# Kernel tuning notes

Measured on AMD Instinct MI355X. Metric: run time of the kernel, lower is better.

## Reference

```python
import jax, jax.numpy as jnp
import numpy as np

N = 100000   # num_nodes
E = 1250000  # num_edges
IN = 64
HID = 64
OUT = 64
LN_EPS = 1e-5


def _gcn_conv(x, src, dst, W, b, n):
    # PyG GCNConv: add self-loops, symmetric deg^{-1/2} normalization, then linear.
    h = x @ W  # (N, out)
    deg = jax.ops.segment_sum(jnp.ones(src.shape[0], h.dtype), dst, num_segments=n) + 1.0  # +1 self-loop
    dinv = jax.lax.rsqrt(deg)
    norm = dinv[src] * dinv[dst]  # (E,)
    out = jax.ops.segment_sum(h[src] * norm[:, None], dst, num_segments=n)
    out = out + h * (dinv * dinv)[:, None]  # self-loop message
    return out + b


def _sage_conv(x, src, dst, Wl, bl, Wr, n):
    # PyG SAGEConv(aggr='mean'): lin_l(mean_{j in N(i)} x_j) + lin_r(x_i); bias only in lin_l.
    cnt = jax.ops.segment_sum(jnp.ones(src.shape[0], x.dtype), dst, num_segments=n)
    agg = jax.ops.segment_sum(x[src], dst, num_segments=n) / jnp.maximum(cnt, 1.0)[:, None]
    return agg @ Wl + bl + x @ Wr


def _layer_norm(x, g, b):
    mu = jnp.mean(x, axis=-1, keepdims=True)
    var = jnp.var(x, axis=-1, keepdims=True)
    return (x - mu) * jax.lax.rsqrt(var + LN_EPS) * g + b


def setup_inputs() -> dict:
    key = jax.random.key(0)
    ks = jax.random.split(key, 16)
    def w(k, shape):
        fan_in = shape[0]
        return (jax.random.normal(k, shape, jnp.float32) / np.sqrt(fan_in)).astype(jnp.float32)
    x = jax.random.normal(ks[0], (N, IN), jnp.float32)
    edge_index = jax.random.randint(ks[1], (2, E), 0, N, dtype=jnp.int64)
    return {
        "x": x,
        "edge_index": edge_index,
        "gcn_w1": w(ks[2], (IN, HID)), "gcn_b1": jnp.zeros((HID,), jnp.float32),
        "gcn_w2": w(ks[3], (HID, OUT)), "gcn_b2": jnp.zeros((OUT,), jnp.float32),
        "sage_wl1": w(ks[4], (IN, HID)), "sage_bl1": jnp.zeros((HID,), jnp.float32),
        "sage_wr1": w(ks[5], (IN, HID)),
        "sage_wl2": w(ks[6], (HID, OUT)), "sage_bl2": jnp.zeros((OUT,), jnp.float32),
        "sage_wr2": w(ks[7], (HID, OUT)),
        "gcn_ln_g": jnp.ones((OUT,), jnp.float32), "gcn_ln_b": jnp.zeros((OUT,), jnp.float32),
        "sage_ln_g": jnp.ones((OUT,), jnp.float32), "sage_ln_b": jnp.zeros((OUT,), jnp.float32),
        "proj_w": w(ks[8], (2 * OUT, OUT)), "proj_b": jnp.zeros((OUT,), jnp.float32),
    }


def reference(x, edge_index, gcn_w1, gcn_b1, gcn_w2, gcn_b2,
              sage_wl1, sage_bl1, sage_wr1, sage_wl2, sage_bl2, sage_wr2,
              gcn_ln_g, gcn_ln_b, sage_ln_g, sage_ln_b, proj_w, proj_b):
    src, dst = edge_index[0], edge_index[1]
    n = x.shape[0]
    # GCN branch (dropout p=0 / eval -> identity)
    g = jax.nn.relu(_gcn_conv(x, src, dst, gcn_w1, gcn_b1, n))
    g = _gcn_conv(g, src, dst, gcn_w2, gcn_b2, n)
    # SAGE branch
    s = jax.nn.relu(_sage_conv(x, src, dst, sage_wl1, sage_bl1, sage_wr1, n))
    s = _sage_conv(s, src, dst, sage_wl2, sage_bl2, sage_wr2, n)
    # Norm + projected-concat fusion
    g = _layer_norm(g, gcn_ln_g, gcn_ln_b)
    s = _layer_norm(s, sage_ln_g, sage_ln_b)
    cat = jnp.concatenate([g, s], axis=-1)  # (N, 2*OUT)
    return cat @ proj_w + proj_b
```

## Files before the change

### kernel.cpp

```cpp
#include <hip/hip_runtime.h>


#define SCAN_CHUNK 2048

typedef __attribute__((ext_vector_type(8))) short short8;
typedef __attribute__((ext_vector_type(4))) short short4v;
typedef __attribute__((ext_vector_type(4))) float floatx4;

__device__ __forceinline__ unsigned short f2bf(float f) {
    unsigned int u = __float_as_uint(f);
    unsigned int r = u + 0x7FFFu + ((u >> 16) & 1u);
    return (unsigned short)(r >> 16);
}
__device__ __forceinline__ float bf2f(unsigned short h) {
    return __uint_as_float(((unsigned int)h) << 16);
}

__global__ void k_count(const int* __restrict__ ei, int E, int* __restrict__ cnt,
                        int* __restrict__ rank) {
    int i = blockIdx.x * blockDim.x + threadIdx.x;
    int e = i * 4;
    if (e + 4 <= E) {
        int4 d = *(const int4*)&ei[E + e];
        int4 r;
        r.x = atomicAdd(&cnt[d.x], 1);
        r.y = atomicAdd(&cnt[d.y], 1);
        r.z = atomicAdd(&cnt[d.z], 1);
        r.w = atomicAdd(&cnt[d.w], 1);
        *(int4*)&rank[e] = r;
    } else {
        for (int j = e; j < E; ++j) rank[j] = atomicAdd(&cnt[ei[E + j]], 1);
    }
}

__global__ void k_scan_reduce(const int* __restrict__ cnt, int N, int* __restrict__ blockSums) {
    __shared__ int lds[256];
    int base = blockIdx.x * SCAN_CHUNK;
    int t = threadIdx.x;
    int s = 0;
    for (int j = 0; j < 8; ++j) {
        int idx = base + t * 8 + j;
        if (idx < N) s += cnt[idx];
    }
    lds[t] = s;
    __syncthreads();
    for (int d = 128; d > 0; d >>= 1) {
        if (t < d) lds[t] += lds[t + d];
        __syncthreads();
    }
    if (t == 0) blockSums[blockIdx.x] = lds[0];
}

__global__ void k_scan_spine(int* __restrict__ blockSums, int B) {
    if (threadIdx.x == 0 && blockIdx.x == 0) {
        int run = 0;
        for (int b = 0; b < B; ++b) { int v = blockSums[b]; blockSums[b] = run; run += v; }
    }
}

__global__ void k_scan_write(const int* __restrict__ cnt, int N,
                             const int* __restrict__ blockSums,
                             int* __restrict__ offs, float* __restrict__ dinv) {
    __shared__ int lds[256];
    int base = blockIdx.x * SCAN_CHUNK;
    int t = threadIdx.x;
    int v[8];
    int s = 0;
    for (int j = 0; j < 8; ++j) {
        int idx = base + t * 8 + j;
        v[j] = (idx < N) ? cnt[idx] : 0;
        s += v[j];
    }
    lds[t] = s;
    __syncthreads();
    for (int d = 1; d < 256; d <<= 1) {
        int x = (t >= d) ? lds[t - d] : 0;
        __syncthreads();
        lds[t] += x;
        __syncthreads();
    }
    int excl = (t == 0) ? 0 : lds[t - 1];
    int run = blockSums[blockIdx.x] + excl;
    for (int j = 0; j < 8; ++j) {
        int idx = base + t * 8 + j;
        if (idx < N) {
            offs[idx] = run;
            run += v[j];
            dinv[idx] = rsqrtf((float)v[j] + 1.0f);
        }
    }
}

__global__ void k_fill(const int* __restrict__ ei, int E, const int* __restrict__ offs,
                       const int* __restrict__ rank, int* __restrict__ csr) {
    int i = blockIdx.x * blockDim.x + threadIdx.x;
    int e = i * 4;
    if (e + 4 <= E) {
        int4 s = *(const int4*)&ei[e];
        int4 d = *(const int4*)&ei[E + e];
        int4 r = *(const int4*)&rank[e];
        csr[offs[d.x] + r.x] = s.x;
        csr[offs[d.y] + r.y] = s.y;
        csr[offs[d.z] + r.z] = s.z;
        csr[offs[d.w] + r.w] = s.w;
    } else {
        for (int j = e; j < E; ++j) csr[offs[ei[E + j]] + rank[j]] = ei[j];
    }
}

__global__ void k_xtobf16(const float* __restrict__ x, unsigned short* __restrict__ xb, int total) {
    int i = blockIdx.x * blockDim.x + threadIdx.x;
    int e = i * 8;
    if (e + 8 <= total) {
        float4 a = *(const float4*)&x[e];
        float4 b = *(const float4*)&x[e + 4];
        short8 o;
        o[0] = (short)f2bf(a.x); o[1] = (short)f2bf(a.y);
        o[2] = (short)f2bf(a.z); o[3] = (short)f2bf(a.w);
        o[4] = (short)f2bf(b.x); o[5] = (short)f2bf(b.y);
        o[6] = (short)f2bf(b.z); o[7] = (short)f2bf(b.w);
        *(short8*)&xb[e] = o;
    } else {
        for (int j = e; j < total; ++j) xb[j] = f2bf(x[j]);
    }
}

__device__ __forceinline__ void xor_reduce8(float4& a, float4& b) {
    a.x += __shfl_xor(a.x, 16, 64); a.y += __shfl_xor(a.y, 16, 64);
    a.z += __shfl_xor(a.z, 16, 64); a.w += __shfl_xor(a.w, 16, 64);
    b.x += __shfl_xor(b.x, 16, 64); b.y += __shfl_xor(b.y, 16, 64);
    b.z += __shfl_xor(b.z, 16, 64); b.w += __shfl_xor(b.w, 16, 64);
    a.x += __shfl_xor(a.x, 32, 64); a.y += __shfl_xor(a.y, 32, 64);
    a.z += __shfl_xor(a.z, 32, 64); a.w += __shfl_xor(a.w, 32, 64);
    b.x += __shfl_xor(b.x, 32, 64); b.y += __shfl_xor(b.y, 32, 64);
    b.z += __shfl_xor(b.z, 32, 64); b.w += __shfl_xor(b.w, 32, 64);
}

__device__ __forceinline__ float red16(float v) {
    v += __shfl_xor(v, 1, 64);
    v += __shfl_xor(v, 2, 64);
    v += __shfl_xor(v, 4, 64);
    v += __shfl_xor(v, 8, 64);
    return v;
}

__global__ void k_gather1_bf(const unsigned short* __restrict__ xb, const int* __restrict__ csr,
                             const int* __restrict__ offs, const int* __restrict__ cnt,
                             const float* __restrict__ dinv,
                             unsigned short* __restrict__ agg, int N) {
    int lane = threadIdx.x & 63;
    int wave = threadIdx.x >> 6;
    int node = blockIdx.x * 4 + wave;
    if (node >= N) return;
    int c = lane & 15, grp = lane >> 4;

    int st = offs[node];
    int cn = cnt[node];
    float di = dinv[node];

    float4 aA = {0.f, 0.f, 0.f, 0.f}, aB = {0.f, 0.f, 0.f, 0.f};
    for (int e = 0; e < cn; e += 8) {
        int i0 = e + grp, i1 = e + 4 + grp;
        float m0 = (i0 < cn) ? 1.f : 0.f;
        float m1 = (i1 < cn) ? 1.f : 0.f;
        int s0 = csr[st + (i0 < cn ? i0 : cn - 1)];
        int s1 = csr[st + (i1 < cn ? i1 : cn - 1)];
        float w0 = m0 * dinv[s0];
        float w1 = m1 * dinv[s1];
        ushort4 u0 = *(const ushort4*)&xb[(size_t)s0 * 64 + 4 * c];
        ushort4 u1 = *(const ushort4*)&xb[(size_t)s1 * 64 + 4 * c];
        float4 v0 = {bf2f(u0.x), bf2f(u0.y), bf2f(u0.z), bf2f(u0.w)};
        float4 v1 = {bf2f(u1.x), bf2f(u1.y), bf2f(u1.z), bf2f(u1.w)};
        aA.x += w0 * v0.x + w1 * v1.x; aA.y += w0 * v0.y + w1 * v1.y;
        aA.z += w0 * v0.z + w1 * v1.z; aA.w += w0 * v0.w + w1 * v1.w;
        aB.x += m0 * v0.x + m1 * v1.x; aB.y += m0 * v0.y + m1 * v1.y;
        aB.z += m0 * v0.z + m1 * v1.z; aB.w += m0 * v0.w + m1 * v1.w;
    }
    xor_reduce8(aA, aB);

    if (grp == 0) {
        ushort4 su = *(const ushort4*)&xb[(size_t)node * 64 + 4 * c];
        float d2 = di * di;
        ushort4 o;
        o.x = f2bf(di * aA.x + d2 * bf2f(su.x));
        o.y = f2bf(di * aA.y + d2 * bf2f(su.y));
        o.z = f2bf(di * aA.z + d2 * bf2f(su.z));
        o.w = f2bf(di * aA.w + d2 * bf2f(su.w));
        *(ushort4*)&agg[(size_t)node * 128 + 4 * c] = o;
    } else if (grp == 1) {
        float rn = 1.0f / fmaxf((float)cn, 1.0f);
        ushort4 o;
        o.x = f2bf(aB.x * rn); o.y = f2bf(aB.y * rn);
        o.z = f2bf(aB.z * rn); o.w = f2bf(aB.w * rn);
        *(ushort4*)&agg[(size_t)node * 128 + 64 + 4 * c] = o;
    }
}

__global__ void k_gather1_f32(const float* __restrict__ x, const int* __restrict__ csr,
                              const int* __restrict__ offs, const int* __restrict__ cnt,
                              const float* __restrict__ dinv,
                              unsigned short* __restrict__ agg, int N) {
    int lane = threadIdx.x & 63;
    int wave = threadIdx.x >> 6;
    int node = blockIdx.x * 4 + wave;
    if (node >= N) return;
    int c = lane & 15, grp = lane >> 4;

    int st = offs[node];
    int cn = cnt[node];
    float di = dinv[node];

    float4 aA = {0.f, 0.f, 0.f, 0.f}, aB = {0.f, 0.f, 0.f, 0.f};
    for (int e = 0; e < cn; e += 8) {
        int i0 = e + grp, i1 = e + 4 + grp;
        float m0 = (i0 < cn) ? 1.f : 0.f;
        float m1 = (i1 < cn) ? 1.f : 0.f;
        int s0 = csr[st + (i0 < cn ? i0 : cn - 1)];
        int s1 = csr[st + (i1 < cn ? i1 : cn - 1)];
        float w0 = m0 * dinv[s0];
        float w1 = m1 * dinv[s1];
        float4 v0 = *(const float4*)&x[(size_t)s0 * 64 + 4 * c];
        float4 v1 = *(const float4*)&x[(size_t)s1 * 64 + 4 * c];
        aA.x += w0 * v0.x + w1 * v1.x; aA.y += w0 * v0.y + w1 * v1.y;
        aA.z += w0 * v0.z + w1 * v1.z; aA.w += w0 * v0.w + w1 * v1.w;
        aB.x += m0 * v0.x + m1 * v1.x; aB.y += m0 * v0.y + m1 * v1.y;
        aB.z += m0 * v0.z + m1 * v1.z; aB.w += m0 * v0.w + m1 * v1.w;
    }
    xor_reduce8(aA, aB);

    if (grp == 0) {
        float4 sq = *(const float4*)&x[(size_t)node * 64 + 4 * c];
        float d2 = di * di;
        ushort4 o;
        o.x = f2bf(di * aA.x + d2 * sq.x); o.y = f2bf(di * aA.y + d2 * sq.y);
        o.z = f2bf(di * aA.z + d2 * sq.z); o.w = f2bf(di * aA.w + d2 * sq.w);
        *(ushort4*)&agg[(size_t)node * 128 + 4 * c] = o;
    } else if (grp == 1) {
        float rn = 1.0f / fmaxf((float)cn, 1.0f);
        ushort4 o;
        o.x = f2bf(aB.x * rn); o.y = f2bf(aB.y * rn);
        o.z = f2bf(aB.z * rn); o.w = f2bf(aB.w * rn);
        *(ushort4*)&agg[(size_t)node * 128 + 64 + 4 * c] = o;
    }
}

__launch_bounds__(512, 1)
__global__ void k_gemm1(const unsigned short* __restrict__ agg,
                        const unsigned short* __restrict__ xb,
                        const float* __restrict__ xf, int use_xb,
                        const float* __restrict__ W1, const float* __restrict__ b1,
                        const float* __restrict__ Wl1, const float* __restrict__ bl1,
                        const float* __restrict__ Wr1,
                        unsigned short* __restrict__ buf1, int N) {
    alignas(16) __shared__ unsigned short sW[3][4096];
    int t = threadIdx.x;
    for (int i = t; i < 1536; i += 512) {
        int m = i >> 9;
        int rem = i & 511;
        int f = rem >> 6;
        int L = rem & 63;
        int kb = (f >> 2) * 32 + (L >> 4) * 8;
        int o = (f & 3) * 16 + (L & 15);
        const float* Wsrc = (m == 0) ? W1 : (m == 1) ? Wl1 : Wr1;
        unsigned short* dst = &sW[m][f * 512 + L * 8];
        #pragma unroll
        for (int j = 0; j < 8; ++j) dst[j] = f2bf(Wsrc[(kb + j) * 64 + o]);
    }
    __syncthreads();

    int lane = t & 63;
    int wave = t >> 6;
    int quad = lane >> 4;
    int n16 = lane & 15;
    int base = blockIdx.x * 128 + wave * 16;
    if (base >= N) return;

    int nm = base + n16;
    if (nm >= N) nm = N - 1;
    const unsigned short* ar = agg + (size_t)nm * 128;

    {
        short8 a0 = *(const short8*)(ar + quad * 8);
        short8 a1 = *(const short8*)(ar + 32 + quad * 8);
        floatx4 g0 = {0.f, 0.f, 0.f, 0.f}, g1 = g0, g2 = g0, g3 = g0;
        g0 = __builtin_amdgcn_mfma_f32_16x16x32_bf16(a0, *(const short8*)&sW[0][0 * 512 + lane * 8], g0, 0, 0, 0);
        g0 = __builtin_amdgcn_mfma_f32_16x16x32_bf16(a1, *(const short8*)&sW[0][4 * 512 + lane * 8], g0, 0, 0, 0);
        g1 = __builtin_amdgcn_mfma_f32_16x16x32_bf16(a0, *(const short8*)&sW[0][1 * 512 + lane * 8], g1, 0, 0, 0);
        g1 = __builtin_amdgcn_mfma_f32_16x16x32_bf16(a1, *(const short8*)&sW[0][5 * 512 + lane * 8], g1, 0, 0, 0);
        g2 = __builtin_amdgcn_mfma_f32_16x16x32_bf16(a0, *(const short8*)&sW[0][2 * 512 + lane * 8], g2, 0, 0, 0);
        g2 = __builtin_amdgcn_mfma_f32_16x16x32_bf16(a1, *(const short8*)&sW[0][6 * 512 + lane * 8], g2, 0, 0, 0);
        g3 = __builtin_amdgcn_mfma_f32_16x16x32_bf16(a0, *(const short8*)&sW[0][3 * 512 + lane * 8], g3, 0, 0, 0);
        g3 = __builtin_amdgcn_mfma_f32_16x16x32_bf16(a1, *(const short8*)&sW[0][7 * 512 + lane * 8], g3, 0, 0, 0);
        floatx4 gt[4] = {g0, g1, g2, g3};
        #pragma unroll
        for (int nt = 0; nt < 4; ++nt) {
            float bg = b1[nt * 16 + n16];
            #pragma unroll
            for (int r = 0; r < 4; ++r) {
                int node = base + quad * 4 + r;
                if (node < N)
                    buf1[(size_t)node * 128 + nt * 16 + n16] = f2bf(fmaxf(gt[nt][r] + bg, 0.f));
            }
        }
    }

    {
        short8 a0 = *(const short8*)(ar + 64 + quad * 8);
        short8 a1 = *(const short8*)(ar + 96 + quad * 8);
        short8 ax0, ax1;
        if (use_xb) {
            ax0 = *(const short8*)&xb[(size_t)nm * 64 + quad * 8];
            ax1 = *(const short8*)&xb[(size_t)nm * 64 + 32 + quad * 8];
        } else {
            float4 xq0 = *(const float4*)&xf[(size_t)nm * 64 + quad * 8];
            float4 xq1 = *(const float4*)&xf[(size_t)nm * 64 + quad * 8 + 4];
            float4 xq2 = *(const float4*)&xf[(size_t)nm * 64 + 32 + quad * 8];
            float4 xq3 = *(const float4*)&xf[(size_t)nm * 64 + 32 + quad * 8 + 4];
            ax0[0] = (short)f2bf(xq0.x); ax0[1] = (short)f2bf(xq0.y);
            ax0[2] = (short)f2bf(xq0.z); ax0[3] = (short)f2bf(xq0.w);
            ax0[4] = (short)f2bf(xq1.x); ax0[5] = (short)f2bf(xq1.y);
            ax0[6] = (short)f2bf(xq1.z); ax0[7] = (short)f2bf(xq1.w);
            ax1[0] = (short)f2bf(xq2.x); ax1[1] = (short)f2bf(xq2.y);
            ax1[2] = (short)f2bf(xq2.z); ax1[3] = (short)f2bf(xq2.w);
            ax1[4] = (short)f2bf(xq3.x); ax1[5] = (short)f2bf(xq3.y);
            ax1[6] = (short)f2bf(xq3.z); ax1[7] = (short)f2bf(xq3.w);
        }

        floatx4 s0 = {0.f, 0.f, 0.f, 0.f}, s1 = s0, s2 = s0, s3 = s0;
        s0 = __builtin_amdgcn_mfma_f32_16x16x32_bf16(a0, *(const short8*)&sW[1][0 * 512 + lane * 8], s0, 0, 0, 0);
        s0 = __builtin_amdgcn_mfma_f32_16x16x32_bf16(a1, *(const short8*)&sW[1][4 * 512 + lane * 8], s0, 0, 0, 0);
        s0 = __builtin_amdgcn_mfma_f32_16x16x32_bf16(ax0, *(const short8*)&sW[2][0 * 512 + lane * 8], s0, 0, 0, 0);
        s0 = __builtin_amdgcn_mfma_f32_16x16x32_bf16(ax1, *(const short8*)&sW[2][4 * 512 + lane * 8], s0, 0, 0, 0);
        s1 = __builtin_amdgcn_mfma_f32_16x16x32_bf16(a0, *(const short8*)&sW[1][1 * 512 + lane * 8], s1, 0, 0, 0);
        s1 = __builtin_amdgcn_mfma_f32_16x16x32_bf16(a1, *(const short8*)&sW[1][5 * 512 + lane * 8], s1, 0, 0, 0);
        s1 = __builtin_amdgcn_mfma_f32_16x16x32_bf16(ax0, *(const short8*)&sW[2][1 * 512 + lane * 8], s1, 0, 0, 0);
        s1 = __builtin_amdgcn_mfma_f32_16x16x32_bf16(ax1, *(const short8*)&sW[2][5 * 512 + lane * 8], s1, 0, 0, 0);
        s2 = __builtin_amdgcn_mfma_f32_16x16x32_bf16(a0, *(const short8*)&sW[1][2 * 512 + lane * 8], s2, 0, 0, 0);
        s2 = __builtin_amdgcn_mfma_f32_16x16x32_bf16(a1, *(const short8*)&sW[1][6 * 512 + lane * 8], s2, 0, 0, 0);
        s2 = __builtin_amdgcn_mfma_f32_16x16x32_bf16(ax0, *(const short8*)&sW[2][2 * 512 + lane * 8], s2, 0, 0, 0);
        s2 = __builtin_amdgcn_mfma_f32_16x16x32_bf16(ax1, *(const short8*)&sW[2][6 * 512 + lane * 8], s2, 0, 0, 0);
        s3 = __builtin_amdgcn_mfma_f32_16x16x32_bf16(a0, *(const short8*)&sW[1][3 * 512 + lane * 8], s3, 0, 0, 0);
        s3 = __builtin_amdgcn_mfma_f32_16x16x32_bf16(a1, *(const short8*)&sW[1][7 * 512 + lane * 8], s3, 0, 0, 0);
        s3 = __builtin_amdgcn_mfma_f32_16x16x32_bf16(ax0, *(const short8*)&sW[2][3 * 512 + lane * 8], s3, 0, 0, 0);
        s3 = __builtin_amdgcn_mfma_f32_16x16x32_bf16(ax1, *(const short8*)&sW[2][7 * 512 + lane * 8], s3, 0, 0, 0);
        floatx4 stl[4] = {s0, s1, s2, s3};
        #pragma unroll
        for (int nt = 0; nt < 4; ++nt) {
            float bs = bl1[nt * 16 + n16];
            #pragma unroll
            for (int r = 0; r < 4; ++r) {
                int node = base + quad * 4 + r;
                if (node < N)
                    buf1[(size_t)node * 128 + 64 + nt * 16 + n16] = f2bf(fmaxf(stl[nt][r] + bs, 0.f));
            }
        }
    }
}

__global__ void k_gather2(const unsigned short* __restrict__ gs, const int* __restrict__ csr,
                          const int* __restrict__ offs, const int* __restrict__ cnt,
                          const float* __restrict__ dinv,
                          unsigned short* __restrict__ agg, int N) {
    int lane = threadIdx.x & 63;
    int wave = threadIdx.x >> 6;
    int node = blockIdx.x * 4 + wave;
    if (node >= N) return;
    int c = lane & 15, grp = lane >> 4;

    int st = offs[node];
    int cn = cnt[node];
    float di = dinv[node];

    float4 aC = {0.f, 0.f, 0.f, 0.f}, aD = {0.f, 0.f, 0.f, 0.f};
    for (int e = 0; e < cn; e += 8) {
        int i0 = e + grp, i1 = e + 4 + grp;
        float m0 = (i0 < cn) ? 1.f : 0.f;
        float m1 = (i1 < cn) ? 1.f : 0.f;
        int s0 = csr[st + (i0 < cn ? i0 : cn - 1)];
        int s1 = csr[st + (i1 < cn ? i1 : cn - 1)];
        float w0 = m0 * dinv[s0];
        float w1 = m1 * dinv[s1];
        const unsigned short* p0 = gs + (size_t)s0 * 128 + 4 * c;
        const unsigned short* p1 = gs + (size_t)s1 * 128 + 4 * c;
        ushort4 g0u = *(const ushort4*)p0;
        ushort4 g1u = *(const ushort4*)p1;
        ushort4 t0u = *(const ushort4*)(p0 + 64);
        ushort4 t1u = *(const ushort4*)(p1 + 64);
        aC.x += w0 * bf2f(g0u.x) + w1 * bf2f(g1u.x);
        aC.y += w0 * bf2f(g0u.y) + w1 * bf2f(g1u.y);
        aC.z += w0 * bf2f(g0u.z) + w1 * bf2f(g1u.z);
        aC.w += w0 * bf2f(g0u.w) + w1 * bf2f(g1u.w);
        aD.x += m0 * bf2f(t0u.x) + m1 * bf2f(t1u.x);
        aD.y += m0 * bf2f(t0u.y) + m1 * bf2f(t1u.y);
        aD.z += m0 * bf2f(t0u.z) + m1 * bf2f(t1u.z);
        aD.w += m0 * bf2f(t0u.w) + m1 * bf2f(t1u.w);
    }
    xor_reduce8(aC, aD);

    if (grp == 0) {
        ushort4 su = *(const ushort4*)&gs[(size_t)node * 128 + 4 * c];
        float d2 = di * di;
        ushort4 o;
        o.x = f2bf(di * aC.x + d2 * bf2f(su.x));
        o.y = f2bf(di * aC.y + d2 * bf2f(su.y));
        o.z = f2bf(di * aC.z + d2 * bf2f(su.z));
        o.w = f2bf(di * aC.w + d2 * bf2f(su.w));
        *(ushort4*)&agg[(size_t)node * 128 + 4 * c] = o;
    } else if (grp == 1) {
        float rn = 1.0f / fmaxf((float)cn, 1.0f);
        ushort4 o;
        o.x = f2bf(aD.x * rn); o.y = f2bf(aD.y * rn);
        o.z = f2bf(aD.z * rn); o.w = f2bf(aD.w * rn);
        *(ushort4*)&agg[(size_t)node * 128 + 64 + 4 * c] = o;
    }
}

__launch_bounds__(512, 1)
__global__ void k_gemm2(const unsigned short* __restrict__ agg,
                        const unsigned short* __restrict__ buf1,
                        const float* __restrict__ W2, const float* __restrict__ b2,
                        const float* __restrict__ Wl2, const float* __restrict__ bl2,
                        const float* __restrict__ Wr2,
                        const float* __restrict__ lngG, const float* __restrict__ lnbG,
                        const float* __restrict__ lngS, const float* __restrict__ lnbS,
                        const float* __restrict__ Pw, const float* __restrict__ Pb,
                        float* __restrict__ out, int N) {
    alignas(16) __shared__ unsigned short sW[3][4096];
    alignas(16) __shared__ unsigned short sP[8192];
    alignas(16) __shared__ unsigned short sT[8][16 * 132];
    int t = threadIdx.x;
    for (int i = t; i < 1536; i += 512) {
        int m = i >> 9;
        int rem = i & 511;
        int f = rem >> 6;
        int L = rem & 63;
        int kb = (f >> 2) * 32 + (L >> 4) * 8;
        int o = (f & 3) * 16 + (L & 15);
        const float* Wsrc = (m == 0) ? W2 : (m == 1) ? Wl2 : Wr2;
        unsigned short* dst = &sW[m][f * 512 + L * 8];
        #pragma unroll
        for (int j = 0; j < 8; ++j) dst[j] = f2bf(Wsrc[(kb + j) * 64 + o]);
    }
    for (int i = t; i < 1024; i += 512) {
        int f = i >> 6;
        int L = i & 63;
        int kb = (f >> 2) * 32 + (L >> 4) * 8;
        int o = (f & 3) * 16 + (L & 15);
        unsigned short* dst = &sP[f * 512 + L * 8];
        #pragma unroll
        for (int j = 0; j < 8; ++j) dst[j] = f2bf(Pw[(kb + j) * 64 + o]);
    }
    __syncthreads();

    int lane = t & 63;
    int wave = t >> 6;
    int quad = lane >> 4;
    int n16 = lane & 15;
    int base = blockIdx.x * 128 + wave * 16;
    if (base >= N) return;
    int nm = base + n16;
    if (nm >= N) nm = N - 1;
    const unsigned short* ar = agg + (size_t)nm * 128;
    const unsigned short* br = buf1 + (size_t)nm * 128;
    unsigned short* tw = &sT[wave][0];

    {
        short8 a0 = *(const short8*)(ar + quad * 8);
        short8 a1 = *(const short8*)(ar + 32 + quad * 8);
        floatx4 c0 = {0.f, 0.f, 0.f, 0.f}, c1 = c0, c2 = c0, c3 = c0;
        c0 = __builtin_amdgcn_mfma_f32_16x16x32_bf16(a0, *(const short8*)&sW[0][0 * 512 + lane * 8], c0, 0, 0, 0);
        c0 = __builtin_amdgcn_mfma_f32_16x16x32_bf16(a1, *(const short8*)&sW[0][4 * 512 + lane * 8], c0, 0, 0, 0);
        c1 = __builtin_amdgcn_mfma_f32_16x16x32_bf16(a0, *(const short8*)&sW[0][1 * 512 + lane * 8], c1, 0, 0, 0);
        c1 = __builtin_amdgcn_mfma_f32_16x16x32_bf16(a1, *(const short8*)&sW[0][5 * 512 + lane * 8], c1, 0, 0, 0);
        c2 = __builtin_amdgcn_mfma_f32_16x16x32_bf16(a0, *(const short8*)&sW[0][2 * 512 + lane * 8], c2, 0, 0, 0);
        c2 = __builtin_amdgcn_mfma_f32_16x16x32_bf16(a1, *(const short8*)&sW[0][6 * 512 + lane * 8], c2, 0, 0, 0);
        c3 = __builtin_amdgcn_mfma_f32_16x16x32_bf16(a0, *(const short8*)&sW[0][3 * 512 + lane * 8], c3, 0, 0, 0);
        c3 = __builtin_amdgcn_mfma_f32_16x16x32_bf16(a1, *(const short8*)&sW[0][7 * 512 + lane * 8], c3, 0, 0, 0);

        float bv0 = b2[n16], bv1 = b2[16 + n16], bv2 = b2[32 + n16], bv3 = b2[48 + n16];
        float gv0 = lngG[n16], gv1 = lngG[16 + n16], gv2 = lngG[32 + n16], gv3 = lngG[48 + n16];
        float ev0 = lnbG[n16], ev1 = lnbG[16 + n16], ev2 = lnbG[32 + n16], ev3 = lnbG[48 + n16];
        #pragma unroll
        for (int r = 0; r < 4; ++r) {
            float z0 = c0[r] + bv0, z1 = c1[r] + bv1, z2 = c2[r] + bv2, z3 = c3[r] + bv3;
            float s = red16(z0 + z1 + z2 + z3);
            float q = red16(z0 * z0 + z1 * z1 + z2 * z2 + z3 * z3);
            float mu = s * (1.0f / 64.0f);
            float var = fmaxf(q * (1.0f / 64.0f) - mu * mu, 0.0f);
            float rs = rsqrtf(var + 1e-5f);
            unsigned short* row = tw + (quad * 4 + r) * 132;
            row[n16]      = f2bf((z0 - mu) * rs * gv0 + ev0);
            row[16 + n16] = f2bf((z1 - mu) * rs * gv1 + ev1);
            row[32 + n16] = f2bf((z2 - mu) * rs * gv2 + ev2);
            row[48 + n16] = f2bf((z3 - mu) * rs * gv3 + ev3);
        }
    }

    {
        short8 a0 = *(const short8*)(ar + 64 + quad * 8);
        short8 a1 = *(const short8*)(ar + 96 + quad * 8);
        short8 v0 = *(const short8*)(br + 64 + quad * 8);
        short8 v1 = *(const short8*)(br + 96 + quad * 8);
        floatx4 c0 = {0.f, 0.f, 0.f, 0.f}, c1 = c0, c2 = c0, c3 = c0;
        c0 = __builtin_amdgcn_mfma_f32_16x16x32_bf16(a0, *(const short8*)&sW[1][0 * 512 + lane * 8], c0, 0, 0, 0);
        c0 = __builtin_amdgcn_mfma_f32_16x16x32_bf16(a1, *(const short8*)&sW[1][4 * 512 + lane * 8], c0, 0, 0, 0);
        c0 = __builtin_amdgcn_mfma_f32_16x16x32_bf16(v0, *(const short8*)&sW[2][0 * 512 + lane * 8], c0, 0, 0, 0);
        c0 = __builtin_amdgcn_mfma_f32_16x16x32_bf16(v1, *(const short8*)&sW[2][4 * 512 + lane * 8], c0, 0, 0, 0);
        c1 = __builtin_amdgcn_mfma_f32_16x16x32_bf16(a0, *(const short8*)&sW[1][1 * 512 + lane * 8], c1, 0, 0, 0);
        c1 = __builtin_amdgcn_mfma_f32_16x16x32_bf16(a1, *(const short8*)&sW[1][5 * 512 + lane * 8], c1, 0, 0, 0);
        c1 = __builtin_amdgcn_mfma_f32_16x16x32_bf16(v0, *(const short8*)&sW[2][1 * 512 + lane * 8], c1, 0, 0, 0);
        c1 = __builtin_amdgcn_mfma_f32_16x16x32_bf16(v1, *(const short8*)&sW[2][5 * 512 + lane * 8], c1, 0, 0, 0);
        c2 = __builtin_amdgcn_mfma_f32_16x16x32_bf16(a0, *(const short8*)&sW[1][2 * 512 + lane * 8], c2, 0, 0, 0);
        c2 = __builtin_amdgcn_mfma_f32_16x16x32_bf16(a1, *(const short8*)&sW[1][6 * 512 + lane * 8], c2, 0, 0, 0);
        c2 = __builtin_amdgcn_mfma_f32_16x16x32_bf16(v0, *(const short8*)&sW[2][2 * 512 + lane * 8], c2, 0, 0, 0);
        c2 = __builtin_amdgcn_mfma_f32_16x16x32_bf16(v1, *(const short8*)&sW[2][6 * 512 + lane * 8], c2, 0, 0, 0);
        c3 = __builtin_amdgcn_mfma_f32_16x16x32_bf16(a0, *(const short8*)&sW[1][3 * 512 + lane * 8], c3, 0, 0, 0);
        c3 = __builtin_amdgcn_mfma_f32_16x16x32_bf16(a1, *(const short8*)&sW[1][7 * 512 + lane * 8], c3, 0, 0, 0);
        c3 = __builtin_amdgcn_mfma_f32_16x16x32_bf16(v0, *(const short8*)&sW[2][3 * 512 + lane * 8], c3, 0, 0, 0);
        c3 = __builtin_amdgcn_mfma_f32_16x16x32_bf16(v1, *(const short8*)&sW[2][7 * 512 + lane * 8], c3, 0, 0, 0);

        float bv0 = bl2[n16], bv1 = bl2[16 + n16], bv2 = bl2[32 + n16], bv3 = bl2[48 + n16];
        float gv0 = lngS[n16], gv1 = lngS[16 + n16], gv2 = lngS[32 + n16], gv3 = lngS[48 + n16];
        float ev0 = lnbS[n16], ev1 = lnbS[16 + n16], ev2 = lnbS[32 + n16], ev3 = lnbS[48 + n16];
        #pragma unroll
        for (int r = 0; r < 4; ++r) {
            float z0 = c0[r] + bv0, z1 = c1[r] + bv1, z2 = c2[r] + bv2, z3 = c3[r] + bv3;
            float s = red16(z0 + z1 + z2 + z3);
            float q = red16(z0 * z0 + z1 * z1 + z2 * z2 + z3 * z3);
            float mu = s * (1.0f / 64.0f);
            float var = fmaxf(q * (1.0f / 64.0f) - mu * mu, 0.0f);
            float rs = rsqrtf(var + 1e-5f);
            unsigned short* row = tw + (quad * 4 + r) * 132 + 64;
            row[n16]      = f2bf((z0 - mu) * rs * gv0 + ev0);
            row[16 + n16] = f2bf((z1 - mu) * rs * gv1 + ev1);
            row[32 + n16] = f2bf((z2 - mu) * rs * gv2 + ev2);
            row[48 + n16] = f2bf((z3 - mu) * rs * gv3 + ev3);
        }
    }

    floatx4 o0 = {0.f, 0.f, 0.f, 0.f}, o1 = o0, o2 = o0, o3 = o0;
    #pragma unroll
    for (int ks = 0; ks < 4; ++ks) {
        const unsigned short* ap = tw + n16 * 132 + ks * 32 + quad * 8;
        short4v lo = *(const short4v*)ap;
        short4v hi = *(const short4v*)(ap + 4);
        short8 af;
        af[0] = lo[0]; af[1] = lo[1]; af[2] = lo[2]; af[3] = lo[3];
        af[4] = hi[0]; af[5] = hi[1]; af[6] = hi[2]; af[7] = hi[3];
        o0 = __builtin_amdgcn_mfma_f32_16x16x32_bf16(af, *(const short8*)&sP[(ks * 4 + 0) * 512 + lane * 8], o0, 0, 0, 0);
        o1 = __builtin_amdgcn_mfma_f32_16x16x32_bf16(af, *(const short8*)&sP[(ks * 4 + 1) * 512 + lane * 8], o1, 0, 0, 0);
        o2 = __builtin_amdgcn_mfma_f32_16x16x32_bf16(af, *(const short8*)&sP[(ks * 4 + 2) * 512 + lane * 8], o2, 0, 0, 0);
        o3 = __builtin_amdgcn_mfma_f32_16x16x32_bf16(af, *(const short8*)&sP[(ks * 4 + 3) * 512 + lane * 8], o3, 0, 0, 0);
    }
    float p0 = Pb[n16], p1 = Pb[16 + n16], p2 = Pb[32 + n16], p3 = Pb[48 + n16];
    floatx4 ot[4] = {o0, o1, o2, o3};
    float pv[4] = {p0, p1, p2, p3};
    #pragma unroll
    for (int nt = 0; nt < 4; ++nt) {
        #pragma unroll
        for (int r = 0; r < 4; ++r) {
            int node = base + quad * 4 + r;
            if (node < N) out[(size_t)node * 64 + nt * 16 + n16] = ot[nt][r] + pv[nt];
        }
    }
}

extern "C" void kernel_launch(void* const* d_in, const int* in_sizes, int n_in,
                              void* d_out, int out_size, void* d_ws, size_t ws_size,
                              hipStream_t stream) {
    const float* x        = (const float*)d_in[0];
    const int*   ei       = (const int*)d_in[1];
    const float* gcn_w1   = (const float*)d_in[2];
    const float* gcn_b1   = (const float*)d_in[3];
    const float* gcn_w2   = (const float*)d_in[4];
    const float* gcn_b2   = (const float*)d_in[5];
    const float* sage_wl1 = (const float*)d_in[6];
    const float* sage_bl1 = (const float*)d_in[7];
    const float* sage_wr1 = (const float*)d_in[8];
    const float* sage_wl2 = (const float*)d_in[9];
    const float* sage_bl2 = (const float*)d_in[10];
    const float* sage_wr2 = (const float*)d_in[11];
    const float* gcn_ln_g = (const float*)d_in[12];
    const float* gcn_ln_b = (const float*)d_in[13];
    const float* sage_ln_g = (const float*)d_in[14];
    const float* sage_ln_b = (const float*)d_in[15];
    const float* proj_w   = (const float*)d_in[16];
    const float* proj_b   = (const float*)d_in[17];
    float* out = (float*)d_out;

    const int N = in_sizes[0] / 64;
    const int E = in_sizes[1] / 2;
    const int B = (N + SCAN_CHUNK - 1) / SCAN_CHUNK;

    char* w = (char*)d_ws;
    size_t off = 0;
    auto alloc = [&](size_t bytes) -> void* {
        void* p = w + off;
        off = (off + bytes + 255) & ~(size_t)255;
        return p;
    };
    int*            cnt       = (int*)alloc((size_t)N * 4);
    int*            offs      = (int*)alloc((size_t)N * 4);
    float*          dinv      = (float*)alloc((size_t)N * 4);
    int*            blockSums = (int*)alloc((size_t)(B + 1) * 4);
    int*            csr       = (int*)alloc((size_t)E * 4);
    unsigned short* agg       = (unsigned short*)alloc((size_t)N * 128 * 2);
    unsigned short* buf1      = (unsigned short*)alloc((size_t)N * 128 * 2);
    size_t off_noxb = off;
    unsigned short* xb        = (unsigned short*)alloc((size_t)N * 64 * 2);
    int use_xb = (off <= ws_size) ? 1 : 0;
    if (!use_xb) off = off_noxb;
    int* rank = (int*)agg;
    (void)n_in; (void)out_size;

    hipMemsetAsync(cnt, 0, (size_t)N * 4, stream);

    int e4Blocks = ((E + 3) / 4 + 255) / 256;
    k_count<<<e4Blocks, 256, 0, stream>>>(ei, E, cnt, rank);
    k_scan_reduce<<<B, 256, 0, stream>>>(cnt, N, blockSums);
    k_scan_spine<<<1, 64, 0, stream>>>(blockSums, B);
    k_scan_write<<<B, 256, 0, stream>>>(cnt, N, blockSums, offs, dinv);
    k_fill<<<e4Blocks, 256, 0, stream>>>(ei, E, offs, rank, csr);

    if (use_xb) {
        int xBlocks = ((N * 64 + 7) / 8 + 255) / 256;
        k_xtobf16<<<xBlocks, 256, 0, stream>>>(x, xb, N * 64);
        k_gather1_bf<<<(N + 3) / 4, 256, 0, stream>>>(xb, csr, offs, cnt, dinv, agg, N);
    } else {
        k_gather1_f32<<<(N + 3) / 4, 256, 0, stream>>>(x, csr, offs, cnt, dinv, agg, N);
    }
    k_gemm1<<<(N + 127) / 128, 512, 0, stream>>>(agg, xb, x, use_xb, gcn_w1, gcn_b1,
                                                 sage_wl1, sage_bl1, sage_wr1, buf1, N);
    k_gather2<<<(N + 3) / 4, 256, 0, stream>>>(buf1, csr, offs, cnt, dinv, agg, N);
    k_gemm2<<<(N + 127) / 128, 512, 0, stream>>>(agg, buf1, gcn_w2, gcn_b2,
                                                 sage_wl2, sage_bl2, sage_wr2,
                                                 gcn_ln_g, gcn_ln_b, sage_ln_g, sage_ln_b,
                                                 proj_w, proj_b, out, N);
}
```

Before: 346.4 us.

## Aggregate neighbor features with MFMA over 16-node tiles using packed edge weights

Replaces the per-node wave-level gather kernels with a kernel that processes 16 destination nodes per wave. Each step stages 32 edges' source rows in LDS, reads them back with transposed LDS reads, and reduces them with bf16 MFMA. The sparse selection matrix comes from a new packed per-edge array holding the local destination id and a precomputed bf16 GCN norm, filled during CSR construction. This is meant to make the gather coalesced across edge ranges and to move the accumulation onto matrix cores. In exchange it adds extra workspace, an extra per-edge array write, and bf16 rounding of the edge norms.

```diff
diff --git a/kernel.cpp b/kernel.cpp
--- a/kernel.cpp
+++ b/kernel.cpp
@@ -14,6 +14,44 @@
 }
 __device__ __forceinline__ float bf2f(unsigned short h) {
     return __uint_as_float(((unsigned int)h) << 16);
+}
+
+__device__ __forceinline__ unsigned lds_addr(const void* p) {
+    return (unsigned)(unsigned long long)(__attribute__((address_space(3))) const char*)p;
+}
+
+__device__ __forceinline__ short8 cat44(short4v lo, short4v hi) {
+    short8 r;
+    r[0] = lo[0]; r[1] = lo[1]; r[2] = lo[2]; r[3] = lo[3];
+    r[4] = hi[0]; r[5] = hi[1]; r[6] = hi[2]; r[7] = hi[3];
+    return r;
+}
+
+template<int NF, int CTB>
+__device__ __forceinline__ void tr_read4(unsigned a0, short8 bf[4]) {
+    short4v l0, h0, l1, h1, l2, h2, l3, h3;
+    asm volatile(
+        "ds_read_b64_tr_b16 %0, %8 offset:%9\n\t"
+        "ds_read_b64_tr_b16 %1, %8 offset:%10\n\t"
+        "ds_read_b64_tr_b16 %2, %8 offset:%11\n\t"
+        "ds_read_b64_tr_b16 %3, %8 offset:%12\n\t"
+        "ds_read_b64_tr_b16 %4, %8 offset:%13\n\t"
+        "ds_read_b64_tr_b16 %5, %8 offset:%14\n\t"
+        "ds_read_b64_tr_b16 %6, %8 offset:%15\n\t"
+        "ds_read_b64_tr_b16 %7, %8 offset:%16\n\t"
+        "s_waitcnt lgkmcnt(0)"
+        : "=&v"(l0), "=&v"(h0), "=&v"(l1), "=&v"(h1),
+          "=&v"(l2), "=&v"(h2), "=&v"(l3), "=&v"(h3)
+        : "v"(a0),
+          "i"((0 * NF + CTB + 0) * 128), "i"((1 * NF + CTB + 0) * 128),
+          "i"((0 * NF + CTB + 1) * 128), "i"((1 * NF + CTB + 1) * 128),
+          "i"((0 * NF + CTB + 2) * 128), "i"((1 * NF + CTB + 2) * 128),
+          "i"((0 * NF + CTB + 3) * 128), "i"((1 * NF + CTB + 3) * 128)
+        : "memory");
+    bf[0] = cat44(l0, h0);
+    bf[1] = cat44(l1, h1);
+    bf[2] = cat44(l2, h2);
+    bf[3] = cat44(l3, h3);
 }
 
 __global__ void k_count(const int* __restrict__ ei, int E, int* __restrict__ cnt,
@@ -87,24 +125,36 @@
             offs[idx] = run;
             run += v[j];
             dinv[idx] = rsqrtf((float)v[j] + 1.0f);
+            if (idx == N - 1) offs[N] = run;
         }
     }
 }
 
 __global__ void k_fill(const int* __restrict__ ei, int E, const int* __restrict__ offs,
-                       const int* __restrict__ rank, int* __restrict__ csr) {
+                       const int* __restrict__ rank, const float* __restrict__ dinv,
+                       int* __restrict__ csr, unsigned int* __restrict__ pk, int use_pk) {
     int i = blockIdx.x * blockDim.x + threadIdx.x;
     int e = i * 4;
     if (e + 4 <= E) {
         int4 s = *(const int4*)&ei[e];
         int4 d = *(const int4*)&ei[E + e];
         int4 r = *(const int4*)&rank[e];
-        csr[offs[d.x] + r.x] = s.x;
-        csr[offs[d.y] + r.y] = s.y;
-        csr[offs[d.z] + r.z] = s.z;
-        csr[offs[d.w] + r.w] = s.w;
+        int p0 = offs[d.x] + r.x, p1 = offs[d.y] + r.y;
+        int p2 = offs[d.z] + r.z, p3 = offs[d.w] + r.w;
+        csr[p0] = s.x; csr[p1] = s.y; csr[p2] = s.z; csr[p3] = s.w;
+        if (use_pk) {
+            pk[p0] = ((unsigned)(d.x & 15) << 16) | f2bf(dinv[s.x] * dinv[d.x]);
+            pk[p1] = ((unsigned)(d.y & 15) << 16) | f2bf(dinv[s.y] * dinv[d.y]);
+            pk[p2] = ((unsigned)(d.z & 15) << 16) | f2bf(dinv[s.z] * dinv[d.z]);
+            pk[p3] = ((unsigned)(d.w & 15) << 16) | f2bf(dinv[s.w] * dinv[d.w]);
+        }
     } else {
-        for (int j = e; j < E; ++j) csr[offs[ei[E + j]] + rank[j]] = ei[j];
+        for (int j = e; j < E; ++j) {
+            int dd = ei[E + j];
+            int p = offs[dd] + rank[j];
+            csr[p] = ei[j];
+            if (use_pk) pk[p] = ((unsigned)(dd & 15) << 16) | f2bf(dinv[ei[j]] * dinv[dd]);
+        }
     }
 }
 
@@ -125,6 +175,137 @@
     }
 }
 
+template<int ROWSH>
+__launch_bounds__(256)
+__global__ void k_gatherM(const unsigned short* __restrict__ feat,
+                          const int* __restrict__ csr,
+                          const unsigned int* __restrict__ pk,
+                          const int* __restrict__ offs, const int* __restrict__ cnt,
+                          const float* __restrict__ dinv,
+                          unsigned short* __restrict__ agg, int N) {
+    constexpr int NF = ROWSH / 16;
+    constexpr int LPR = ROWSH / 8;
+    constexpr int EPP = 64 / LPR;
+    constexpr int PASSES = 32 / EPP;
+
+    __shared__ unsigned short sbuf[4 * 32 * ROWSH];
+
+    const int lane = threadIdx.x & 63;
+    const int wave = threadIdx.x >> 6;
+    const int base = blockIdx.x * 64 + wave * 16;
+    if (base >= N) return;
+
+    unsigned short* wb = &sbuf[wave * 32 * ROWSH];
+    const unsigned wboff = lds_addr(wb);
+    const int q = lane >> 4;
+    const int d16 = lane & 15;
+
+    const int se = lane / LPR;
+    const int sf = (lane % LPR) * 8;
+    const int sf_sub = sf >> 4;
+    const int sf_lo = sf & 15;
+
+    const int elo = offs[base];
+    const int ehi = offs[min(base + 16, N)];
+
+    floatx4 accg[4], accs[4];
+#pragma unroll
+    for (int i = 0; i < 4; ++i) {
+        accg[i] = floatx4{0.f, 0.f, 0.f, 0.f};
+        accs[i] = floatx4{0.f, 0.f, 0.f, 0.f};
+    }
+
+    const unsigned a0 = wboff + (unsigned)(q * 2 * NF) * 128u + (unsigned)d16 * 8u;
+
+    for (int k0 = elo; k0 < ehi; k0 += 32) {
+        short8 stg[PASSES];
+#pragma unroll
+        for (int p = 0; p < PASSES; ++p) {
+            int idx = k0 + p * EPP + se;
+            int src = csr[idx < ehi ? idx : ehi - 1];
+            stg[p] = *(const short8*)&feat[(size_t)src * ROWSH + sf];
+        }
+        int i0 = k0 + q * 8;
+        short8 aG, aS;
+#pragma unroll
+        for (int j = 0; j < 8; ++j) {
+            unsigned u = pk[i0 + j];
+            bool ok = ((int)(u >> 16) == d16) && (i0 + j < ehi);
+            aG[j] = ok ? (short)(u & 0xffffu) : (short)0;
+            aS[j] = ok ? (short)0x3F80 : (short)0;
+        }
+#pragma unroll
+        for (int p = 0; p < PASSES; ++p) {
+            int e = p * EPP + se;
+            int elem = ((e >> 2) * NF + sf_sub) * 64 + (e & 3) * 16 + sf_lo;
+            *(short8*)&wb[elem] = stg[p];
+        }
+        asm volatile("s_waitcnt lgkmcnt(0)" ::: "memory");
+        __builtin_amdgcn_sched_barrier(0);
+
+        short8 bG[4];
+        tr_read4<NF, 0>(a0, bG);
+#pragma unroll
+        for (int ct = 0; ct < 4; ++ct)
+            accg[ct] = __builtin_amdgcn_mfma_f32_16x16x32_bf16(aG, bG[ct], accg[ct], 0, 0, 0);
+        if constexpr (NF == 8) {
+            short8 bS[4];
+            tr_read4<NF, 4>(a0, bS);
+#pragma unroll
+            for (int ct = 0; ct < 4; ++ct)
+                accs[ct] = __builtin_amdgcn_mfma_f32_16x16x32_bf16(aS, bS[ct], accs[ct], 0, 0, 0);
+        } else {
+#pragma unroll
+            for (int ct = 0; ct < 4; ++ct)
+                accs[ct] = __builtin_amdgcn_mfma_f32_16x16x32_bf16(aS, bG[ct], accs[ct], 0, 0, 0);
+        }
+    }
+
+    {
+        short8 stg[PASSES];
+#pragma unroll
+        for (int p = 0; p < PASSES; ++p) {
+            int nd = base + p * EPP + se;
+            if (nd >= N) nd = N - 1;
+            stg[p] = *(const short8*)&feat[(size_t)nd * ROWSH + sf];
+        }
+        float ds = dinv[min(base + d16, N - 1)];
+        unsigned short wself = f2bf(ds * ds);
+        short8 aG;
+#pragma unroll
+        for (int j = 0; j < 8; ++j) {
+            bool ok = ((q * 8 + j) == d16) && (base + d16 < N);
+            aG[j] = ok ? (short)wself : (short)0;
+        }
+#pragma unroll
+        for (int p = 0; p < PASSES; ++p) {
+            int e = p * EPP + se;
+            int elem = ((e >> 2) * NF + sf_sub) * 64 + (e & 3) * 16 + sf_lo;
+            *(short8*)&wb[elem] = stg[p];
+        }
+        asm volatile("s_waitcnt lgkmcnt(0)" ::: "memory");
+        __builtin_amdgcn_sched_barrier(0);
+        short8 bG[4];
+        tr_read4<NF, 0>(a0, bG);
+#pragma unroll
+        for (int ct = 0; ct < 4; ++ct)
+            accg[ct] = __builtin_amdgcn_mfma_f32_16x16x32_bf16(aG, bG[ct], accg[ct], 0, 0, 0);
+    }
+
+#pragma unroll
+    for (int r = 0; r < 4; ++r) {
+        int node = base + q * 4 + r;
+        if (node < N) {
+            float rn = 1.0f / fmaxf((float)cnt[node], 1.0f);
+#pragma unroll
+            for (int ct = 0; ct < 4; ++ct) {
+                agg[(size_t)node * 128 + ct * 16 + d16]      = f2bf(accg[ct][r]);
+                agg[(size_t)node * 128 + 64 + ct * 16 + d16] = f2bf(accs[ct][r] * rn);
+            }
+        }
+    }
+}
+
 __device__ __forceinline__ void xor_reduce8(float4& a, float4& b) {
     a.x += __shfl_xor(a.x, 16, 64); a.y += __shfl_xor(a.y, 16, 64);
     a.z += __shfl_xor(a.z, 16, 64); a.w += __shfl_xor(a.w, 16, 64);
@@ -142,58 +323,6 @@
     v += __shfl_xor(v, 4, 64);
     v += __shfl_xor(v, 8, 64);
     return v;
-}
-
-__global__ void k_gather1_bf(const unsigned short* __restrict__ xb, const int* __restrict__ csr,
-                             const int* __restrict__ offs, const int* __restrict__ cnt,
-                             const float* __restrict__ dinv,
-                             unsigned short* __restrict__ agg, int N) {
-    int lane = threadIdx.x & 63;
-    int wave = threadIdx.x >> 6;
-    int node = blockIdx.x * 4 + wave;
-    if (node >= N) return;
-    int c = lane & 15, grp = lane >> 4;
-
-    int st = offs[node];
-    int cn = cnt[node];
-    float di = dinv[node];
-
-    float4 aA = {0.f, 0.f, 0.f, 0.f}, aB = {0.f, 0.f, 0.f, 0.f};
-    for (int e = 0; e < cn; e += 8) {
-        int i0 = e + grp, i1 = e + 4 + grp;
-        float m0 = (i0 < cn) ? 1.f : 0.f;
-        float m1 = (i1 < cn) ? 1.f : 0.f;
-        int s0 = csr[st + (i0 < cn ? i0 : cn - 1)];
-        int s1 = csr[st + (i1 < cn ? i1 : cn - 1)];
-        float w0 = m0 * dinv[s0];
-        float w1 = m1 * dinv[s1];
-        ushort4 u0 = *(const ushort4*)&xb[(size_t)s0 * 64 + 4 * c];
-        ushort4 u1 = *(const ushort4*)&xb[(size_t)s1 * 64 + 4 * c];
-        float4 v0 = {bf2f(u0.x), bf2f(u0.y), bf2f(u0.z), bf2f(u0.w)};
-        float4 v1 = {bf2f(u1.x), bf2f(u1.y), bf2f(u1.z), bf2f(u1.w)};
-        aA.x += w0 * v0.x + w1 * v1.x; aA.y += w0 * v0.y + w1 * v1.y;
-        aA.z += w0 * v0.z + w1 * v1.z; aA.w += w0 * v0.w + w1 * v1.w;
-        aB.x += m0 * v0.x + m1 * v1.x; aB.y += m0 * v0.y + m1 * v1.y;
-        aB.z += m0 * v0.z + m1 * v1.z; aB.w += m0 * v0.w + m1 * v1.w;
-    }
-    xor_reduce8(aA, aB);
-
-    if (grp == 0) {
-        ushort4 su = *(const ushort4*)&xb[(size_t)node * 64 + 4 * c];
-        float d2 = di * di;
-        ushort4 o;
-        o.x = f2bf(di * aA.x + d2 * bf2f(su.x));
-        o.y = f2bf(di * aA.y + d2 * bf2f(su.y));
-        o.z = f2bf(di * aA.z + d2 * bf2f(su.z));
-        o.w = f2bf(di * aA.w + d2 * bf2f(su.w));
-        *(ushort4*)&agg[(size_t)node * 128 + 4 * c] = o;
-    } else if (grp == 1) {
-        float rn = 1.0f / fmaxf((float)cn, 1.0f);
-        ushort4 o;
-        o.x = f2bf(aB.x * rn); o.y = f2bf(aB.y * rn);
-        o.z = f2bf(aB.z * rn); o.w = f2bf(aB.w * rn);
-        *(ushort4*)&agg[(size_t)node * 128 + 64 + 4 * c] = o;
-    }
 }
 
 __global__ void k_gather1_f32(const float* __restrict__ x, const int* __restrict__ csr,
@@ -240,6 +369,64 @@
         ushort4 o;
         o.x = f2bf(aB.x * rn); o.y = f2bf(aB.y * rn);
         o.z = f2bf(aB.z * rn); o.w = f2bf(aB.w * rn);
+        *(ushort4*)&agg[(size_t)node * 128 + 64 + 4 * c] = o;
+    }
+}
+
+__global__ void k_gather2(const unsigned short* __restrict__ gs, const int* __restrict__ csr,
+                          const int* __restrict__ offs, const int* __restrict__ cnt,
+                          const float* __restrict__ dinv,
+                          unsigned short* __restrict__ agg, int N) {
+    int lane = threadIdx.x & 63;
+    int wave = threadIdx.x >> 6;
+    int node = blockIdx.x * 4 + wave;
+    if (node >= N) return;
+    int c = lane & 15, grp = lane >> 4;
+
+    int st = offs[node];
+    int cn = cnt[node];
+    float di = dinv[node];
+
+    float4 aC = {0.f, 0.f, 0.f, 0.f}, aD = {0.f, 0.f, 0.f, 0.f};
+    for (int e = 0; e < cn; e += 8) {
+        int i0 = e + grp, i1 = e + 4 + grp;
+        float m0 = (i0 < cn) ? 1.f : 0.f;
+        float m1 = (i1 < cn) ? 1.f : 0.f;
+        int s0 = csr[st + (i0 < cn ? i0 : cn - 1)];
+        int s1 = csr[st + (i1 < cn ? i1 : cn - 1)];
+        float w0 = m0 * dinv[s0];
+        float w1 = m1 * dinv[s1];
+        const unsigned short* p0 = gs + (size_t)s0 * 128 + 4 * c;
+        const unsigned short* p1 = gs + (size_t)s1 * 128 + 4 * c;
+        ushort4 g0u = *(const ushort4*)p0;
+        ushort4 g1u = *(const ushort4*)p1;
+        ushort4 t0u = *(const ushort4*)(p0 + 64);
+        ushort4 t1u = *(const ushort4*)(p1 + 64);
+        aC.x += w0 * bf2f(g0u.x) + w1 * bf2f(g1u.x);
+        aC.y += w0 * bf2f(g0u.y) + w1 * bf2f(g1u.y);
+        aC.z += w0 * bf2f(g0u.z) + w1 * bf2f(g1u.z);
+        aC.w += w0 * bf2f(g0u.w) + w1 * bf2f(g1u.w);
+        aD.x += m0 * bf2f(t0u.x) + m1 * bf2f(t1u.x);
+        aD.y += m0 * bf2f(t0u.y) + m1 * bf2f(t1u.y);
+        aD.z += m0 * bf2f(t0u.z) + m1 * bf2f(t1u.z);
+        aD.w += m0 * bf2f(t0u.w) + m1 * bf2f(t1u.w);
+    }
+    xor_reduce8(aC, aD);
+
+    if (grp == 0) {
+        ushort4 su = *(const ushort4*)&gs[(size_t)node * 128 + 4 * c];
+        float d2 = di * di;
+        ushort4 o;
+        o.x = f2bf(di * aC.x + d2 * bf2f(su.x));
+        o.y = f2bf(di * aC.y + d2 * bf2f(su.y));
+        o.z = f2bf(di * aC.z + d2 * bf2f(su.z));
+        o.w = f2bf(di * aC.w + d2 * bf2f(su.w));
+        *(ushort4*)&agg[(size_t)node * 128 + 4 * c] = o;
+    } else if (grp == 1) {
+        float rn = 1.0f / fmaxf((float)cn, 1.0f);
+        ushort4 o;
+        o.x = f2bf(aD.x * rn); o.y = f2bf(aD.y * rn);
+        o.z = f2bf(aD.z * rn); o.w = f2bf(aD.w * rn);
         *(ushort4*)&agg[(size_t)node * 128 + 64 + 4 * c] = o;
     }
 }
@@ -357,64 +544,6 @@
     }
 }
 
-__global__ void k_gather2(const unsigned short* __restrict__ gs, const int* __restrict__ csr,
-                          const int* __restrict__ offs, const int* __restrict__ cnt,
-                          const float* __restrict__ dinv,
-                          unsigned short* __restrict__ agg, int N) {
-    int lane = threadIdx.x & 63;
-    int wave = threadIdx.x >> 6;
-    int node = blockIdx.x * 4 + wave;
-    if (node >= N) return;
-    int c = lane & 15, grp = lane >> 4;
-
-    int st = offs[node];
-    int cn = cnt[node];
-    float di = dinv[node];
-
-    float4 aC = {0.f, 0.f, 0.f, 0.f}, aD = {0.f, 0.f, 0.f, 0.f};
-    for (int e = 0; e < cn; e += 8) {
-        int i0 = e + grp, i1 = e + 4 + grp;
-        float m0 = (i0 < cn) ? 1.f : 0.f;
-        float m1 = (i1 < cn) ? 1.f : 0.f;
-        int s0 = csr[st + (i0 < cn ? i0 : cn - 1)];
-        int s1 = csr[st + (i1 < cn ? i1 : cn - 1)];
-        float w0 = m0 * dinv[s0];
-        float w1 = m1 * dinv[s1];
-        const unsigned short* p0 = gs + (size_t)s0 * 128 + 4 * c;
-        const unsigned short* p1 = gs + (size_t)s1 * 128 + 4 * c;
-        ushort4 g0u = *(const ushort4*)p0;
-        ushort4 g1u = *(const ushort4*)p1;
-        ushort4 t0u = *(const ushort4*)(p0 + 64);
-        ushort4 t1u = *(const ushort4*)(p1 + 64);
-        aC.x += w0 * bf2f(g0u.x) + w1 * bf2f(g1u.x);
-        aC.y += w0 * bf2f(g0u.y) + w1 * bf2f(g1u.y);
-        aC.z += w0 * bf2f(g0u.z) + w1 * bf2f(g1u.z);
-        aC.w += w0 * bf2f(g0u.w) + w1 * bf2f(g1u.w);
-        aD.x += m0 * bf2f(t0u.x) + m1 * bf2f(t1u.x);
-        aD.y += m0 * bf2f(t0u.y) + m1 * bf2f(t1u.y);
-        aD.z += m0 * bf2f(t0u.z) + m1 * bf2f(t1u.z);
-        aD.w += m0 * bf2f(t0u.w) + m1 * bf2f(t1u.w);
-    }
-    xor_reduce8(aC, aD);
-
-    if (grp == 0) {
-        ushort4 su = *(const ushort4*)&gs[(size_t)node * 128 + 4 * c];
-        float d2 = di * di;
-        ushort4 o;
-        o.x = f2bf(di * aC.x + d2 * bf2f(su.x));
-        o.y = f2bf(di * aC.y + d2 * bf2f(su.y));
-        o.z = f2bf(di * aC.z + d2 * bf2f(su.z));
-        o.w = f2bf(di * aC.w + d2 * bf2f(su.w));
-        *(ushort4*)&agg[(size_t)node * 128 + 4 * c] = o;
-    } else if (grp == 1) {
-        float rn = 1.0f / fmaxf((float)cn, 1.0f);
-        ushort4 o;
-        o.x = f2bf(aD.x * rn); o.y = f2bf(aD.y * rn);
-        o.z = f2bf(aD.z * rn); o.w = f2bf(aD.w * rn);
-        *(ushort4*)&agg[(size_t)node * 128 + 64 + 4 * c] = o;
-    }
-}
-
 __launch_bounds__(512, 1)
 __global__ void k_gemm2(const unsigned short* __restrict__ agg,
                         const unsigned short* __restrict__ buf1,
@@ -600,16 +729,17 @@
         return p;
     };
     int*            cnt       = (int*)alloc((size_t)N * 4);
-    int*            offs      = (int*)alloc((size_t)N * 4);
+    int*            offs      = (int*)alloc((size_t)(N + 1) * 4);
     float*          dinv      = (float*)alloc((size_t)N * 4);
     int*            blockSums = (int*)alloc((size_t)(B + 1) * 4);
-    int*            csr       = (int*)alloc((size_t)E * 4);
+    int*            csr       = (int*)alloc((size_t)(E + 32) * 4);
     unsigned short* agg       = (unsigned short*)alloc((size_t)N * 128 * 2);
     unsigned short* buf1      = (unsigned short*)alloc((size_t)N * 128 * 2);
-    size_t off_noxb = off;
+    size_t off_nonew = off;
+    unsigned int*   pk        = (unsigned int*)alloc((size_t)(E + 32) * 4);
     unsigned short* xb        = (unsigned short*)alloc((size_t)N * 64 * 2);
-    int use_xb = (off <= ws_size) ? 1 : 0;
-    if (!use_xb) off = off_noxb;
+    int use_new = (off <= ws_size) ? 1 : 0;
+    if (!use_new) off = off_nonew;
     int* rank = (int*)agg;
     (void)n_in; (void)out_size;
 
@@ -620,18 +750,21 @@
     k_scan_reduce<<<B, 256, 0, stream>>>(cnt, N, blockSums);
     k_scan_spine<<<1, 64, 0, stream>>>(blockSums, B);
     k_scan_write<<<B, 256, 0, stream>>>(cnt, N, blockSums, offs, dinv);
-    k_fill<<<e4Blocks, 256, 0, stream>>>(ei, E, offs, rank, csr);
-
-    if (use_xb) {
+    k_fill<<<e4Blocks, 256, 0, stream>>>(ei, E, offs, rank, dinv, csr, pk, use_new);
+
+    if (use_new) {
         int xBlocks = ((N * 64 + 7) / 8 + 255) / 256;
         k_xtobf16<<<xBlocks, 256, 0, stream>>>(x, xb, N * 64);
-        k_gather1_bf<<<(N + 3) / 4, 256, 0, stream>>>(xb, csr, offs, cnt, dinv, agg, N);
+        k_gatherM<64><<<(N + 63) / 64, 256, 0, stream>>>(xb, csr, pk, offs, cnt, dinv, agg, N);
+        k_gemm1<<<(N + 127) / 128, 512, 0, stream>>>(agg, xb, x, 1, gcn_w1, gcn_b1,
+                                                     sage_wl1, sage_bl1, sage_wr1, buf1, N);
+        k_gatherM<128><<<(N + 63) / 64, 256, 0, stream>>>(buf1, csr, pk, offs, cnt, dinv, agg, N);
     } else {
         k_gather1_f32<<<(N + 3) / 4, 256, 0, stream>>>(x, csr, offs, cnt, dinv, agg, N);
-    }
-    k_gemm1<<<(N + 127) / 128, 512, 0, stream>>>(agg, xb, x, use_xb, gcn_w1, gcn_b1,
-                                                 sage_wl1, sage_bl1, sage_wr1, buf1, N);
-    k_gather2<<<(N + 3) / 4, 256, 0, stream>>>(buf1, csr, offs, cnt, dinv, agg, N);
+        k_gemm1<<<(N + 127) / 128, 512, 0, stream>>>(agg, xb, x, 0, gcn_w1, gcn_b1,
+                                                     sage_wl1, sage_bl1, sage_wr1, buf1, N);
+        k_gather2<<<(N + 3) / 4, 256, 0, stream>>>(buf1, csr, offs, cnt, dinv, agg, N);
+    }
     k_gemm2<<<(N + 127) / 128, 512, 0, stream>>>(agg, buf1, gcn_w2, gcn_b2,
                                                  sage_wl2, sage_bl2, sage_wr2,
                                                  gcn_ln_g, gcn_ln_b, sage_ln_g, sage_ln_b,
```

Result: no change. 342.0 us (-1.3%).
